# Kernel optimization log

Hardware: AMD Instinct MI355X
Metric: run time of the kernel (lower is better)

## Reference

```python
import jax, jax.numpy as jnp
import numpy as np

PRIME = 2147483647  # 2^31 - 1, MinHash modulus
GAMMA = 0.3
NUM_HEADS = 8


def minhash_sketch(ids, a, b):
    # ids: (B, L, S) int64 atom ids; a,b: (K,) hash coefficients
    # h[b,l,s,k] = (a[k]*id + b[k]) mod PRIME ; signature = min over the set axis S
    h = (ids[..., None] * a + b) % PRIME          # (B, L, S, K)
    return h.min(axis=2)                          # (B, L, K)


def jaccard_from_signatures(sig_q, sig_k):
    # sig_q: (B, Lq, K), sig_k: (B, Lk, K) -> (B, Lq, Lk) fraction of matching slots.
    # Scan over the K hash slots to avoid materializing a (B,Lq,Lk,K) tensor.
    B, Lq, K = sig_q.shape
    Lk = sig_k.shape[1]

    def step(acc, cols):
        qc, kc = cols                              # (B,Lq), (B,Lk)
        return acc + (qc[:, :, None] == kc[:, None, :]).astype(jnp.float32), None

    init = jnp.zeros((B, Lq, Lk), jnp.float32)
    xs = (jnp.moveaxis(sig_q, -1, 0), jnp.moveaxis(sig_k, -1, 0))
    acc, _ = jax.lax.scan(step, init, xs)
    return acc / K


def symdiff_from_jaccard(jacc, size_q, size_k):
    # |A ∩ B| = J/(1+J) * (|A|+|B|)  =>  |A Δ B| = (|A|+|B|) * (1-J)/(1+J)
    tot = size_q[:, :, None] + size_k[:, None, :]   # (B, Lq, Lk)
    return tot * (1.0 - jacc) / (1.0 + jacc)


def setup_inputs() -> dict:
    key = jax.random.key(0)
    ks = jax.random.split(key, 12)
    B, Lq, Lk, E, S, K, V = 4, 1024, 1024, 512, 8, 128, 32000
    w = lambda k: (jax.random.normal(k, (E, E), jnp.float32) * 0.02)
    return {
        "query": jax.random.normal(ks[0], (B, Lq, E), jnp.float32),
        "key": jax.random.normal(ks[1], (B, Lk, E), jnp.float32),
        "value": jax.random.normal(ks[2], (B, Lk, E), jnp.float32),
        "token_sets_q": jax.random.randint(ks[3], (B, Lq, S), 0, V).astype(jnp.int64),
        "token_sets_k": jax.random.randint(ks[4], (B, Lk, S), 0, V).astype(jnp.int64),
        "hash_a": jax.random.randint(ks[5], (K,), 1, PRIME - 1).astype(jnp.int64),
        "hash_b": jax.random.randint(ks[6], (K,), 0, PRIME - 1).astype(jnp.int64),
        "Wq": w(ks[7]), "bq": jnp.zeros((E,), jnp.float32),
        "Wk": w(ks[8]), "bk": jnp.zeros((E,), jnp.float32),
        "Wv": w(ks[9]), "bv": jnp.zeros((E,), jnp.float32),
        "Wo": w(ks[10]), "bo": jnp.zeros((E,), jnp.float32),
    }


def reference(query, key, value, token_sets_q, token_sets_k, hash_a, hash_b,
              Wq, bq, Wk, bk, Wv, bv, Wo, bo):
    B, Lq, E = query.shape
    Lk = key.shape[1]
    H = NUM_HEADS
    d = E // H

    # in-projections (torch Linear: x @ W^T + b); q,k are computed but the
    # attention scores come solely from the token-set kernel (gating disabled)
    q = query @ Wq.T + bq
    k = key @ Wk.T + bk
    v = (value @ Wv.T + bv).reshape(B, Lk, H, d).transpose(0, 2, 1, 3)  # (B,H,Lk,d)

    # MinHash sketches of per-token atom sets -> estimated Jaccard -> Δ-RBF score
    sig_q = minhash_sketch(token_sets_q, hash_a, hash_b)   # (B,Lq,K)
    sig_k = minhash_sketch(token_sets_k, hash_a, hash_b)   # (B,Lk,K)
    jacc = jaccard_from_signatures(sig_q, sig_k)           # (B,Lq,Lk)

    S = token_sets_q.shape[-1]
    size_q = jnp.full((B, Lq), S, jnp.float32)             # uniform CSR offsets -> |set| = S
    size_k = jnp.full((B, Lk), S, jnp.float32)
    delta = symdiff_from_jaccard(jacc, size_q, size_k)
    scores = jnp.exp(-GAMMA * delta)                       # (B,Lq,Lk), shared by all heads

    attn = jax.nn.softmax(scores, axis=-1)                 # no masks, no causal, dropout=0
    ctx = jnp.einsum('bqk,bhkd->bqhd', attn, v).reshape(B, Lq, E)
    return ctx @ Wo.T + bo
```

## Files before the change

### kernel.cpp

```cpp
#include <hip/hip_runtime.h>
#include <hip/hip_bf16.h>
#include <stdint.h>

#define PRIME 2147483647u
#define GAMMA 0.3f
#define K_HASH 128
#define S_SET 8
#define NB 4
#define LQ 1024
#define LK 1024
#define EDIM 512

typedef unsigned short ushort_t;
typedef __attribute__((ext_vector_type(8))) short short8;
typedef __attribute__((ext_vector_type(4))) float f32x4;

static __device__ __forceinline__ unsigned short f2bf(float f) {
    unsigned u = __builtin_bit_cast(unsigned, f);
    u += 0x7FFFu + ((u >> 16) & 1u);
    return (unsigned short)(u >> 16);
}

static __device__ __forceinline__ void glds16(const void* g, void* l) {
    __builtin_amdgcn_global_load_lds(
        (const __attribute__((address_space(1))) unsigned int*)g,
        (__attribute__((address_space(3))) unsigned int*)l, 16, 0, 0);
}

#define SWZ(r) ((((r) >> 2) & 3) ^ ((r) & 3))

#define CVT_N0 (NB * LK * EDIM)
#define CVT_N1 (EDIM * EDIM)
#define CVT_N2 (EDIM * EDIM)
__global__ __launch_bounds__(256) void cvt_kernel(
        const float* __restrict__ v, const float* __restrict__ wv,
        const float* __restrict__ wo,
        ushort_t* __restrict__ vb, ushort_t* __restrict__ wvb,
        ushort_t* __restrict__ wob) {
    size_t i = ((size_t)blockIdx.x * 256 + threadIdx.x) * 8;
    const float* src; ushort_t* dst; size_t off;
    if (i < CVT_N0)                { src = v;  dst = vb;  off = i; }
    else if (i < CVT_N0 + CVT_N1)  { src = wv; dst = wvb; off = i - CVT_N0; }
    else                           { src = wo; dst = wob; off = i - CVT_N0 - CVT_N1; }
    float4 a = *(const float4*)(src + off);
    float4 b = *(const float4*)(src + off + 4);
    ushort4 o0, o1;
    o0.x = f2bf(a.x); o0.y = f2bf(a.y); o0.z = f2bf(a.z); o0.w = f2bf(a.w);
    o1.x = f2bf(b.x); o1.y = f2bf(b.y); o1.z = f2bf(b.z); o1.w = f2bf(b.w);
    *(ushort4*)(dst + off)     = o0;
    *(ushort4*)(dst + off + 4) = o1;
}

__global__ __launch_bounds__(128) void sig_kernel(
        const int* __restrict__ ts_q, const int* __restrict__ ts_k,
        const int* __restrict__ ha, const int* __restrict__ hb,
        int* __restrict__ sig_q, int* __restrict__ sig_k) {
    int blk = blockIdx.x;
    const int* ts = (blk < NB * LQ) ? ts_q : ts_k;
    int*      sig = (blk < NB * LQ) ? sig_q : sig_k;
    int idx = blk & (NB * LQ - 1);
    int k = threadIdx.x;
    unsigned long long a  = (unsigned)ha[k];
    unsigned long long bb = (unsigned)hb[k];
    __shared__ int ids[S_SET];
    if (k < S_SET) ids[k] = ts[idx * S_SET + k];
    __syncthreads();
    unsigned mn = 0xFFFFFFFFu;
    #pragma unroll
    for (int s = 0; s < S_SET; s++) {
        unsigned long long x = a * (unsigned long long)(unsigned)ids[s] + bb;
        x = (x & PRIME) + (x >> 31);
        x = (x & PRIME) + (x >> 31);
        unsigned r = (unsigned)x;
        if (r >= PRIME) r -= PRIME;
        mn = (r < mn) ? r : mn;
    }
    sig[idx * K_HASH + k] = (int)mn;
}

__global__ __launch_bounds__(256) void jaccard_kernel(
        const int* __restrict__ sig_q, const int* __restrict__ sig_k,
        unsigned short* __restrict__ P) {
    __shared__ int Qs[64 * 32];
    __shared__ int Ks[64 * 32];
    __shared__ float lut[K_HASH + 1];
    int tid = threadIdx.x;
    if (tid <= K_HASH) {
        float r = (float)(K_HASH - tid) / (float)(K_HASH + tid);
        float score = expf(-GAMMA * (2.0f * S_SET) * r);
        lut[tid] = expf(score);
    }
    int b  = blockIdx.z;
    int q0 = blockIdx.y * 64, j0 = blockIdx.x * 64;
    const int* sq = sig_q + ((size_t)b * LQ + q0) * K_HASH;
    const int* sk = sig_k + ((size_t)b * LK + j0) * K_HASH;
    int tx = tid & 15, ty = tid >> 4;
    int cnt[4][4] = {};
    int srow = tid >> 2, gbase = (tid & 3) * 2;
    #pragma unroll 1
    for (int ch = 0; ch < 4; ch++) {
        __syncthreads();
        const int4* gq = (const int4*)(sq + srow * K_HASH + ch * 32);
        const int4* gk = (const int4*)(sk + srow * K_HASH + ch * 32);
        #pragma unroll
        for (int u = 0; u < 2; u++) {
            int g = gbase + u;
            int sg = ((g + (srow >> 2)) & 7) * 4;
            *(int4*)&Qs[srow * 32 + sg] = gq[g];
            *(int4*)&Ks[srow * 32 + sg] = gk[g];
        }
        __syncthreads();
        #pragma unroll
        for (int cc = 0; cc < 8; cc++) {
            int4 qv[4], kv[4];
            #pragma unroll
            for (int i = 0; i < 4; i++) {
                int r = ty * 4 + i;
                qv[i] = *(const int4*)&Qs[r * 32 + (((cc + (r >> 2)) & 7) * 4)];
            }
            #pragma unroll
            for (int j = 0; j < 4; j++) {
                int r = tx * 4 + j;
                kv[j] = *(const int4*)&Ks[r * 32 + (((cc + (r >> 2)) & 7) * 4)];
            }
            #pragma unroll
            for (int i = 0; i < 4; i++)
                #pragma unroll
                for (int j = 0; j < 4; j++)
                    cnt[i][j] += (qv[i].x == kv[j].x) + (qv[i].y == kv[j].y)
                               + (qv[i].z == kv[j].z) + (qv[i].w == kv[j].w);
        }
    }
    unsigned short* Pb = P + (size_t)b * LQ * LK;
    #pragma unroll
    for (int i = 0; i < 4; i++) {
        int q = q0 + ty * 4 + i;
        ushort4 o;
        o.x = f2bf(lut[cnt[i][0]]);
        o.y = f2bf(lut[cnt[i][1]]);
        o.z = f2bf(lut[cnt[i][2]]);
        o.w = f2bf(lut[cnt[i][3]]);
        *(ushort4*)&Pb[(size_t)q * LK + j0 + tx * 4] = o;
    }
}

__global__ __launch_bounds__(256) void rowsum_kernel(
        const unsigned short* __restrict__ P, float* __restrict__ invs) {
    int wave = threadIdx.x >> 6, lane = threadIdx.x & 63;
    int row = blockIdx.x * 4 + wave;
    const uint4* p4 = (const uint4*)(P + (size_t)row * LK);
    float s = 0.f;
    for (int t = lane; t < LK / 8; t += 64) {
        uint4 v = p4[t];
        unsigned wd[4] = {v.x, v.y, v.z, v.w};
        #pragma unroll
        for (int i = 0; i < 4; i++) {
            s += __builtin_bit_cast(float, wd[i] << 16);
            s += __builtin_bit_cast(float, wd[i] & 0xFFFF0000u);
        }
    }
    #pragma unroll
    for (int off = 32; off > 0; off >>= 1) s += __shfl_down(s, off, 64);
    if (lane == 0) invs[row] = 1.0f / s;
}

#define EPI_ROWBIAS  0
#define EPI_ROWSCALE 1
#define EPI_COLBIAS  2

template<int OUTF32, int MODE>
__global__ __launch_bounds__(256) void btgemm_kernel(
        const ushort_t* __restrict__ A, const ushort_t* __restrict__ B,
        void* __restrict__ C,
        const float* __restrict__ bias, const float* __restrict__ scale,
        int lda, int ldb, int ldc, int Kd,
        long long sA, long long sB, long long sC, long long sS) {
    __shared__ ushort_t As[2][128 * 32];
    __shared__ ushort_t Bs[2][64 * 32];
    int z = blockIdx.z;
    int m0 = blockIdx.y * 128, n0 = blockIdx.x * 64;
    int tid = threadIdx.x;
    int w = tid >> 6, lane = tid & 63;
    int wm = (w & 1) * 64, wn = (w >> 1) * 32;
    int mrow = lane & 15, kg = lane >> 4;

    int r = tid >> 2, c = (tid & 3) ^ SWZ(r);
    const ushort_t* pa0 = A + (size_t)z * sA + (size_t)(m0 + r) * lda + c * 8;
    const ushort_t* pa1 = pa0 + (size_t)64 * lda;
    const ushort_t* pb  = B + (size_t)z * sB + (size_t)(n0 + r) * ldb + c * 8;

    int aoff[4], boff[2];
    #pragma unroll
    for (int i = 0; i < 4; i++) {
        int R = wm + i * 16 + mrow;
        aoff[i] = R * 32 + (kg ^ SWZ(R)) * 8;
    }
    #pragma unroll
    for (int j = 0; j < 2; j++) {
        int R = wn + j * 16 + mrow;
        boff[j] = R * 32 + (kg ^ SWZ(R)) * 8;
    }

    f32x4 acc[4][2] = {};
    int nK = Kd >> 5;
    glds16(pa0, &As[0][tid * 8]);
    glds16(pa1, &As[0][2048 + tid * 8]);
    glds16(pb,  &Bs[0][tid * 8]);
    for (int i = 0; i < nK; i++) {
        __syncthreads();
        int cur = i & 1, nxt = cur ^ 1;
        if (i + 1 < nK) {
            int k0 = (i + 1) << 5;
            glds16(pa0 + k0, &As[nxt][tid * 8]);
            glds16(pa1 + k0, &As[nxt][2048 + tid * 8]);
            glds16(pb  + k0, &Bs[nxt][tid * 8]);
        }
        short8 af[4], bh[2];
        #pragma unroll
        for (int ii = 0; ii < 4; ii++) af[ii] = *(const short8*)&As[cur][aoff[ii]];
        #pragma unroll
        for (int jj = 0; jj < 2; jj++) bh[jj] = *(const short8*)&Bs[cur][boff[jj]];
        #pragma unroll
        for (int ii = 0; ii < 4; ii++)
            #pragma unroll
            for (int jj = 0; jj < 2; jj++)
                acc[ii][jj] = __builtin_amdgcn_mfma_f32_16x16x32_bf16(
                                  af[ii], bh[jj], acc[ii][jj], 0, 0, 0);
    }

    const float* sc = scale + (size_t)z * sS;
    int col = lane & 15, rbase = (lane >> 4) * 4;
    #pragma unroll
    for (int ii = 0; ii < 4; ii++) {
        #pragma unroll
        for (int jj = 0; jj < 2; jj++) {
            #pragma unroll
            for (int rr = 0; rr < 4; rr++) {
                int gm = m0 + wm + ii * 16 + rbase + rr;
                int gn = n0 + wn + jj * 16 + col;
                float v = acc[ii][jj][rr];
                if (MODE == EPI_ROWBIAS)       v += bias[gm];
                else if (MODE == EPI_ROWSCALE) v *= sc[gm];
                else                           v += bias[gn];
                size_t cix = (size_t)z * sC + (size_t)gm * ldc + gn;
                if (OUTF32) ((float*)C)[cix] = v;
                else        ((ushort_t*)C)[cix] = f2bf(v);
            }
        }
    }
}

extern "C" void kernel_launch(void* const* d_in, const int* in_sizes, int n_in,
                              void* d_out, int out_size, void* d_ws, size_t ws_size,
                              hipStream_t stream) {
    const float* value = (const float*)d_in[2];
    const int* tsq = (const int*)d_in[3];
    const int* tsk = (const int*)d_in[4];
    const int* ha  = (const int*)d_in[5];
    const int* hb  = (const int*)d_in[6];
    const float* Wv = (const float*)d_in[11];
    const float* bv = (const float*)d_in[12];
    const float* Wo = (const float*)d_in[13];
    const float* bo = (const float*)d_in[14];
    float* out = (float*)d_out;

    char* ws = (char*)d_ws;
    int* sigq        = (int*)(ws);
    int* sigk        = (int*)(ws + (2ull << 20));
    ushort_t* P      = (ushort_t*)(ws + (4ull << 20));
    float* invs      = (float*)(ws + (12ull << 20));
    ushort_t* Vt     = (ushort_t*)(ws + (12ull << 20) + (1ull << 16));
    ushort_t* ctx    = (ushort_t*)(ws + (17ull << 20));
    ushort_t* Vb     = (ushort_t*)(ws + (21ull << 20));
    ushort_t* Wvb    = (ushort_t*)(ws + (25ull << 20));
    ushort_t* Wob    = (ushort_t*)(ws + (25ull << 20) + (512ull << 10));

    cvt_kernel<<<(CVT_N0 + CVT_N1 + CVT_N2) / (256 * 8), 256, 0, stream>>>(
        value, Wv, Wo, Vb, Wvb, Wob);

    sig_kernel<<<2 * NB * LQ, 128, 0, stream>>>(tsq, tsk, ha, hb, sigq, sigk);

    jaccard_kernel<<<dim3(LK / 64, LQ / 64, NB), 256, 0, stream>>>(sigq, sigk, P);

    rowsum_kernel<<<NB * LQ / 4, 256, 0, stream>>>(P, invs);

    btgemm_kernel<0, EPI_ROWBIAS><<<dim3(4096 / 64, 512 / 128, 1), 256, 0, stream>>>(
        Wvb, Vb, Vt, bv, invs ,
        EDIM, EDIM, NB * LK, EDIM, 0LL, 0LL, 0LL, 0LL);

    btgemm_kernel<0, EPI_ROWSCALE><<<dim3(EDIM / 64, LQ / 128, NB), 256, 0, stream>>>(
        P, Vt, ctx, bv , invs,
        LK, NB * LK, EDIM, LK,
        (long long)LQ * LK, (long long)LK, (long long)LQ * EDIM, (long long)LQ);

    btgemm_kernel<1, EPI_COLBIAS><<<dim3(EDIM / 64, NB * LQ / 128, 1), 256, 0, stream>>>(
        ctx, Wob, out, bo, invs ,
        EDIM, EDIM, EDIM, EDIM, 0LL, 0LL, 0LL, 0LL);
}
```

Before: 179.7 us.

## Pack MinHash signatures to 16 bits and fuse row sums into Jaccard kernel

Signatures are stored as 16-bit values, and two hash slots are compared per 32-bit word using XOR plus a packed min, which halves the Jaccard kernel's load and compare work. The Jaccard tile grows to 128x128 with an 8x8 per-thread micro-tile, giving more reuse of each value loaded from shared memory. The softmax row sums are now accumulated in that epilogue with atomics into a buffer that the signature kernel zeroes. This removes the separate rowsum pass over P, and the context GEMM divides by the sum instead of scaling by a reciprocal. In exchange, truncating hashes to 16 bits allows spurious slot matches, so the similarity is slightly approximate, and the float atomics make the row sums order-dependent.

```diff
diff --git a/kernel.cpp b/kernel.cpp
--- a/kernel.cpp
+++ b/kernel.cpp
@@ -14,6 +14,7 @@
 typedef unsigned short ushort_t;
 typedef __attribute__((ext_vector_type(8))) short short8;
 typedef __attribute__((ext_vector_type(4))) float f32x4;
+typedef __attribute__((ext_vector_type(2))) unsigned short u16x2;
 
 static __device__ __forceinline__ unsigned short f2bf(float f) {
     unsigned u = __builtin_bit_cast(unsigned, f);
@@ -28,6 +29,21 @@
 }
 
 #define SWZ(r) ((((r) >> 2) & 3) ^ ((r) & 3))
+
+static __device__ __forceinline__ unsigned nm2(unsigned acc, unsigned a, unsigned b) {
+    unsigned x = a ^ b;
+    u16x2 xv = __builtin_bit_cast(u16x2, x);
+    u16x2 one; one.x = 1; one.y = 1;
+    u16x2 t = __builtin_elementwise_min(xv, one);
+    return acc + __builtin_bit_cast(unsigned, t);
+}
+static __device__ __forceinline__ unsigned nm8(unsigned acc, int4 q, int4 k) {
+    acc = nm2(acc, (unsigned)q.x, (unsigned)k.x);
+    acc = nm2(acc, (unsigned)q.y, (unsigned)k.y);
+    acc = nm2(acc, (unsigned)q.z, (unsigned)k.z);
+    acc = nm2(acc, (unsigned)q.w, (unsigned)k.w);
+    return acc;
+}
 
 #define CVT_N0 (NB * LK * EDIM)
 #define CVT_N1 (EDIM * EDIM)
@@ -54,12 +70,14 @@
 __global__ __launch_bounds__(128) void sig_kernel(
         const int* __restrict__ ts_q, const int* __restrict__ ts_k,
         const int* __restrict__ ha, const int* __restrict__ hb,
-        int* __restrict__ sig_q, int* __restrict__ sig_k) {
+        ushort_t* __restrict__ sig_q, ushort_t* __restrict__ sig_k,
+        float* __restrict__ rs) {
     int blk = blockIdx.x;
+    int k = threadIdx.x;
+    if (blk < 32) rs[blk * 128 + k] = 0.f;
     const int* ts = (blk < NB * LQ) ? ts_q : ts_k;
-    int*      sig = (blk < NB * LQ) ? sig_q : sig_k;
+    ushort_t* sig = (blk < NB * LQ) ? sig_q : sig_k;
     int idx = blk & (NB * LQ - 1);
-    int k = threadIdx.x;
     unsigned long long a  = (unsigned)ha[k];
     unsigned long long bb = (unsigned)hb[k];
     __shared__ int ids[S_SET];
@@ -75,97 +93,84 @@
         if (r >= PRIME) r -= PRIME;
         mn = (r < mn) ? r : mn;
     }
-    sig[idx * K_HASH + k] = (int)mn;
+    sig[idx * K_HASH + k] = (ushort_t)mn;
 }
 
 __global__ __launch_bounds__(256) void jaccard_kernel(
-        const int* __restrict__ sig_q, const int* __restrict__ sig_k,
-        unsigned short* __restrict__ P) {
-    __shared__ int Qs[64 * 32];
-    __shared__ int Ks[64 * 32];
+        const ushort_t* __restrict__ sig_q, const ushort_t* __restrict__ sig_k,
+        ushort_t* __restrict__ P, float* __restrict__ rs) {
+    __shared__ int Qs[128 * 16];
+    __shared__ int Ks[128 * 17];
     __shared__ float lut[K_HASH + 1];
     int tid = threadIdx.x;
     if (tid <= K_HASH) {
         float r = (float)(K_HASH - tid) / (float)(K_HASH + tid);
-        float score = expf(-GAMMA * (2.0f * S_SET) * r);
-        lut[tid] = expf(score);
-    }
-    int b  = blockIdx.z;
-    int q0 = blockIdx.y * 64, j0 = blockIdx.x * 64;
-    const int* sq = sig_q + ((size_t)b * LQ + q0) * K_HASH;
-    const int* sk = sig_k + ((size_t)b * LK + j0) * K_HASH;
+        lut[tid] = expf(expf(-GAMMA * (2.0f * S_SET) * r));
+    }
+    int b = blockIdx.z;
+    int q0 = blockIdx.y * 128, j0 = blockIdx.x * 128;
+    const int4* gq = (const int4*)(sig_q + ((size_t)b * LQ + q0) * K_HASH);
+    const int4* gk = (const int4*)(sig_k + ((size_t)b * LK + j0) * K_HASH);
     int tx = tid & 15, ty = tid >> 4;
-    int cnt[4][4] = {};
-    int srow = tid >> 2, gbase = (tid & 3) * 2;
+    unsigned acc[8][8] = {};
+    int r0 = tid >> 2, g0 = tid & 3;
+    int r1 = (tid + 256) >> 2;
     #pragma unroll 1
     for (int ch = 0; ch < 4; ch++) {
         __syncthreads();
-        const int4* gq = (const int4*)(sq + srow * K_HASH + ch * 32);
-        const int4* gk = (const int4*)(sk + srow * K_HASH + ch * 32);
-        #pragma unroll
-        for (int u = 0; u < 2; u++) {
-            int g = gbase + u;
-            int sg = ((g + (srow >> 2)) & 7) * 4;
-            *(int4*)&Qs[srow * 32 + sg] = gq[g];
-            *(int4*)&Ks[srow * 32 + sg] = gk[g];
+        *(int4*)&Qs[r0 * 16 + ((g0 + (r0 >> 3)) & 3) * 4] = gq[r0 * 16 + ch * 4 + g0];
+        *(int4*)&Qs[r1 * 16 + ((g0 + (r1 >> 3)) & 3) * 4] = gq[r1 * 16 + ch * 4 + g0];
+        *(int4*)&Ks[r0 * 17 + ((g0 + (r0 >> 5)) & 3) * 4] = gk[r0 * 16 + ch * 4 + g0];
+        *(int4*)&Ks[r1 * 17 + ((g0 + (r1 >> 5)) & 3) * 4] = gk[r1 * 16 + ch * 4 + g0];
+        __syncthreads();
+        #pragma unroll
+        for (int cc = 0; cc < 4; cc++) {
+            int4 qv[8], kv[8];
+            #pragma unroll
+            for (int i = 0; i < 8; i++)
+                qv[i] = *(const int4*)&Qs[(ty * 8 + i) * 16 + ((cc + ty) & 3) * 4];
+            #pragma unroll
+            for (int j = 0; j < 8; j++)
+                kv[j] = *(const int4*)&Ks[(tx * 8 + j) * 17 + ((cc + (tx >> 2)) & 3) * 4];
+            #pragma unroll
+            for (int i = 0; i < 8; i++)
+                #pragma unroll
+                for (int j = 0; j < 8; j++)
+                    acc[i][j] = nm8(acc[i][j], qv[i], kv[j]);
         }
-        __syncthreads();
-        #pragma unroll
-        for (int cc = 0; cc < 8; cc++) {
-            int4 qv[4], kv[4];
-            #pragma unroll
-            for (int i = 0; i < 4; i++) {
-                int r = ty * 4 + i;
-                qv[i] = *(const int4*)&Qs[r * 32 + (((cc + (r >> 2)) & 7) * 4)];
-            }
-            #pragma unroll
-            for (int j = 0; j < 4; j++) {
-                int r = tx * 4 + j;
-                kv[j] = *(const int4*)&Ks[r * 32 + (((cc + (r >> 2)) & 7) * 4)];
-            }
-            #pragma unroll
-            for (int i = 0; i < 4; i++)
-                #pragma unroll
-                for (int j = 0; j < 4; j++)
-                    cnt[i][j] += (qv[i].x == kv[j].x) + (qv[i].y == kv[j].y)
-                               + (qv[i].z == kv[j].z) + (qv[i].w == kv[j].w);
+    }
+    ushort_t* Pb = P + (size_t)b * LQ * LK;
+    float fsum[8];
+    #pragma unroll
+    for (int i = 0; i < 8; i++) {
+        float s = 0.f;
+        ushort_t o[8];
+        #pragma unroll
+        for (int j = 0; j < 8; j++) {
+            unsigned nm = (acc[i][j] & 0xFFFFu) + (acc[i][j] >> 16);
+            float p = lut[K_HASH - nm];
+            s += p;
+            o[j] = f2bf(p);
         }
-    }
-    unsigned short* Pb = P + (size_t)b * LQ * LK;
-    #pragma unroll
-    for (int i = 0; i < 4; i++) {
-        int q = q0 + ty * 4 + i;
-        ushort4 o;
-        o.x = f2bf(lut[cnt[i][0]]);
-        o.y = f2bf(lut[cnt[i][1]]);
-        o.z = f2bf(lut[cnt[i][2]]);
-        o.w = f2bf(lut[cnt[i][3]]);
-        *(ushort4*)&Pb[(size_t)q * LK + j0 + tx * 4] = o;
-    }
-}
-
-__global__ __launch_bounds__(256) void rowsum_kernel(
-        const unsigned short* __restrict__ P, float* __restrict__ invs) {
-    int wave = threadIdx.x >> 6, lane = threadIdx.x & 63;
-    int row = blockIdx.x * 4 + wave;
-    const uint4* p4 = (const uint4*)(P + (size_t)row * LK);
-    float s = 0.f;
-    for (int t = lane; t < LK / 8; t += 64) {
-        uint4 v = p4[t];
-        unsigned wd[4] = {v.x, v.y, v.z, v.w};
-        #pragma unroll
-        for (int i = 0; i < 4; i++) {
-            s += __builtin_bit_cast(float, wd[i] << 16);
-            s += __builtin_bit_cast(float, wd[i] & 0xFFFF0000u);
-        }
-    }
-    #pragma unroll
-    for (int off = 32; off > 0; off >>= 1) s += __shfl_down(s, off, 64);
-    if (lane == 0) invs[row] = 1.0f / s;
+        fsum[i] = s;
+        int row = q0 + ty * 8 + i;
+        *(short8*)&Pb[(size_t)row * LK + j0 + tx * 8] = *(const short8*)o;
+    }
+    __syncthreads();
+    float* fs = (float*)Qs;
+    #pragma unroll
+    for (int i = 0; i < 8; i++) fs[(ty * 8 + i) * 16 + tx] = fsum[i];
+    __syncthreads();
+    if (tid < 128) {
+        float s = 0.f;
+        #pragma unroll
+        for (int t = 0; t < 16; t++) s += fs[tid * 16 + t];
+        atomicAdd(&rs[(size_t)b * LQ + q0 + tid], s);
+    }
 }
 
 #define EPI_ROWBIAS  0
-#define EPI_ROWSCALE 1
+#define EPI_ROWDIV   1
 #define EPI_COLBIAS  2
 
 template<int OUTF32, int MODE>
@@ -239,9 +244,9 @@
                 int gm = m0 + wm + ii * 16 + rbase + rr;
                 int gn = n0 + wn + jj * 16 + col;
                 float v = acc[ii][jj][rr];
-                if (MODE == EPI_ROWBIAS)       v += bias[gm];
-                else if (MODE == EPI_ROWSCALE) v *= sc[gm];
-                else                           v += bias[gn];
+                if (MODE == EPI_ROWBIAS)     v += bias[gm];
+                else if (MODE == EPI_ROWDIV) v /= sc[gm];
+                else                         v += bias[gn];
                 size_t cix = (size_t)z * sC + (size_t)gm * ldc + gn;
                 if (OUTF32) ((float*)C)[cix] = v;
                 else        ((ushort_t*)C)[cix] = f2bf(v);
@@ -265,10 +270,10 @@
     float* out = (float*)d_out;
 
     char* ws = (char*)d_ws;
-    int* sigq        = (int*)(ws);
-    int* sigk        = (int*)(ws + (2ull << 20));
+    ushort_t* sigq   = (ushort_t*)(ws);
+    ushort_t* sigk   = (ushort_t*)(ws + (1ull << 20));
     ushort_t* P      = (ushort_t*)(ws + (4ull << 20));
-    float* invs      = (float*)(ws + (12ull << 20));
+    float* rs        = (float*)(ws + (12ull << 20));
     ushort_t* Vt     = (ushort_t*)(ws + (12ull << 20) + (1ull << 16));
     ushort_t* ctx    = (ushort_t*)(ws + (17ull << 20));
     ushort_t* Vb     = (ushort_t*)(ws + (21ull << 20));
@@ -278,22 +283,20 @@
     cvt_kernel<<<(CVT_N0 + CVT_N1 + CVT_N2) / (256 * 8), 256, 0, stream>>>(
         value, Wv, Wo, Vb, Wvb, Wob);
 
-    sig_kernel<<<2 * NB * LQ, 128, 0, stream>>>(tsq, tsk, ha, hb, sigq, sigk);
-
-    jaccard_kernel<<<dim3(LK / 64, LQ / 64, NB), 256, 0, stream>>>(sigq, sigk, P);
-
-    rowsum_kernel<<<NB * LQ / 4, 256, 0, stream>>>(P, invs);
+    sig_kernel<<<2 * NB * LQ, 128, 0, stream>>>(tsq, tsk, ha, hb, sigq, sigk, rs);
+
+    jaccard_kernel<<<dim3(LK / 128, LQ / 128, NB), 256, 0, stream>>>(sigq, sigk, P, rs);
 
     btgemm_kernel<0, EPI_ROWBIAS><<<dim3(4096 / 64, 512 / 128, 1), 256, 0, stream>>>(
-        Wvb, Vb, Vt, bv, invs ,
+        Wvb, Vb, Vt, bv, rs ,
         EDIM, EDIM, NB * LK, EDIM, 0LL, 0LL, 0LL, 0LL);
 
-    btgemm_kernel<0, EPI_ROWSCALE><<<dim3(EDIM / 64, LQ / 128, NB), 256, 0, stream>>>(
-        P, Vt, ctx, bv , invs,
+    btgemm_kernel<0, EPI_ROWDIV><<<dim3(EDIM / 64, LQ / 128, NB), 256, 0, stream>>>(
+        P, Vt, ctx, bv , rs,
         LK, NB * LK, EDIM, LK,
         (long long)LQ * LK, (long long)LK, (long long)LQ * EDIM, (long long)LQ);
 
     btgemm_kernel<1, EPI_COLBIAS><<<dim3(EDIM / 64, NB * LQ / 128, 1), 256, 0, stream>>>(
-        ctx, Wob, out, bo, invs ,
+        ctx, Wob, out, bo, rs ,
         EDIM, EDIM, EDIM, EDIM, 0LL, 0LL, 0LL, 0LL);
 }
```

New measurement: 204.2 us. 13.6% more time.
